# Performance work log

Hardware: AMD Instinct MI355X
Metric: run time of the kernel (lower is better)

## Reference

```python
import jax, jax.numpy as jnp
import numpy as np
import math

B, TD, TP, D, H = 16, 256, 1024, 512, 8
DH = D // H
G_MIN = 0.05
LN_EPS = 1e-5
SCALE = 1.0 / math.sqrt(DH)


def _ln(x, g, b):
    m = jnp.mean(x, axis=-1, keepdims=True)
    v = jnp.var(x, axis=-1, keepdims=True)
    return (x - m) * jax.lax.rsqrt(v + LN_EPS) * g + b


def _evi(x, w1, b1, w2, b2, k):
    # EvidentialHead: Linear -> SiLU -> Linear(d->4), NIG params -> gate
    h = jax.nn.silu(x @ w1 + b1)
    p = h @ w2 + b2  # (B,T,4)
    gamma, nu, alpha, beta = jnp.split(p, 4, axis=-1)
    nu = jax.nn.softplus(nu) + 1e-6
    alpha = jax.nn.softplus(alpha) + 1.0
    beta = jax.nn.softplus(beta) + 1e-6
    sigma2 = beta / (nu * (alpha - 1.0))  # (B,T,1)
    g = jnp.clip(jnp.exp(-k * sigma2[..., 0]), G_MIN, 1.0)  # (B,T)
    return g


def _xattn(Q, KV, log_bias, wq, bq, wk, bk, wv, bv, wo, bo, lng, lnb):
    # Q: (B,M,D), KV: (B,N,D), log_bias: (B,N) added to logits pre-softmax
    Bq, M, _ = Q.shape
    N = KV.shape[1]
    q = (Q @ wq + bq).reshape(Bq, M, H, DH)
    k_ = (KV @ wk + bk).reshape(Bq, N, H, DH)
    v = (KV @ wv + bv).reshape(Bq, N, H, DH)
    scores = jnp.einsum('bmhd,bnhd->bhmn', q, k_) * SCALE
    scores = scores + log_bias[:, None, None, :]
    attn = jax.nn.softmax(scores, axis=-1)
    out = jnp.einsum('bhmn,bnhd->bmhd', attn, v).reshape(Bq, M, D)
    out = out @ wo + bo
    return _ln(Q + out, lng, lnb)


def _ffn(x, w1, b1, w2, b2, lng, lnb):
    # Linear(d,4d) -> SiLU -> Linear(4d,d) -> LayerNorm (no residual)
    h = jax.nn.silu(x @ w1 + b1)
    return _ln(h @ w2 + b2, lng, lnb)


def setup_inputs() -> dict:
    key = jax.random.key(0)
    ks = iter(jax.random.split(key, 64))

    def w(shape, s=0.02):
        return s * jax.random.normal(next(ks), shape, jnp.float32)

    def attn_params(pfx):
        p = {}
        for nm in ('wq', 'wk', 'wv', 'wo'):
            p[pfx + '_' + nm] = w((D, D))
        for nm in ('bq', 'bk', 'bv', 'bo'):
            p[pfx + '_' + nm] = jnp.zeros((D,), jnp.float32)
        p[pfx + '_lng'] = jnp.ones((D,), jnp.float32)
        p[pfx + '_lnb'] = jnp.zeros((D,), jnp.float32)
        return p

    def ffn_params(pfx):
        return {pfx + '_w1': w((D, 4 * D)), pfx + '_b1': jnp.zeros((4 * D,), jnp.float32),
                pfx + '_w2': w((4 * D, D)), pfx + '_b2': jnp.zeros((D,), jnp.float32),
                pfx + '_lng': jnp.ones((D,), jnp.float32), pfx + '_lnb': jnp.zeros((D,), jnp.float32)}

    inp = {
        'Hd': jax.random.normal(next(ks), (B, TD, D), jnp.float32),
        'Hp': jax.random.normal(next(ks), (B, TP, D), jnp.float32),
        'k': 1,
        'evid_w1': w((D, D)), 'evid_b1': jnp.zeros((D,), jnp.float32),
        'evid_w2': w((D, 4)), 'evid_b2': jnp.zeros((4,), jnp.float32),
        'evip_w1': w((D, D)), 'evip_b1': jnp.zeros((D,), jnp.float32),
        'evip_w2': w((D, 4)), 'evip_b2': jnp.zeros((4,), jnp.float32),
    }
    inp.update(attn_params('p2d'))
    inp.update(attn_params('d2p'))
    inp.update(ffn_params('ffnd'))
    inp.update(ffn_params('ffnp'))
    return inp


def reference(Hd, Hp, k,
              evid_w1, evid_b1, evid_w2, evid_b2,
              evip_w1, evip_b1, evip_w2, evip_b2,
              p2d_wq, p2d_wk, p2d_wv, p2d_wo, p2d_bq, p2d_bk, p2d_bv, p2d_bo, p2d_lng, p2d_lnb,
              d2p_wq, d2p_wk, d2p_wv, d2p_wo, d2p_bq, d2p_bk, d2p_bv, d2p_bo, d2p_lng, d2p_lnb,
              ffnd_w1, ffnd_b1, ffnd_w2, ffnd_b2, ffnd_lng, ffnd_lnb,
              ffnp_w1, ffnp_b1, ffnp_w2, ffnp_b2, ffnp_lng, ffnp_lnb):
    gd = _evi(Hd, evid_w1, evid_b1, evid_w2, evid_b2, k)  # (B,TD)
    gp = _evi(Hp, evip_w1, evip_b1, evip_w2, evip_b2, k)  # (B,TP)
    Hp2 = _xattn(Hp, Hd, jnp.log(gd + 1e-12),
                 p2d_wq, p2d_bq, p2d_wk, p2d_bk, p2d_wv, p2d_bv, p2d_wo, p2d_bo, p2d_lng, p2d_lnb)
    Hd2 = _xattn(Hd, Hp, jnp.log(gp + 1e-12),
                 d2p_wq, d2p_bq, d2p_wk, d2p_bk, d2p_wv, d2p_bv, d2p_wo, d2p_bo, d2p_lng, d2p_lnb)
    Hd_out = _ffn(Hd2, ffnd_w1, ffnd_b1, ffnd_w2, ffnd_b2, ffnd_lng, ffnd_lnb)
    Hp_out = _ffn(Hp2, ffnp_w1, ffnp_b1, ffnp_w2, ffnp_b2, ffnp_lng, ffnp_lnb)
    return (Hd_out, Hp_out, gd, gp)
```

## Files before the change

kernel.cpp:

```cpp
#include <hip/hip_runtime.h>
#include <stdint.h>
#include <math.h>

typedef unsigned short u16;
typedef __attribute__((ext_vector_type(8))) short bf16x8;
typedef __attribute__((ext_vector_type(8))) short short8;
typedef __attribute__((ext_vector_type(4))) float f32x4;
typedef __attribute__((ext_vector_type(4))) unsigned short u16x4;

#define NB 16
#define TDr 256
#define TPr 1024
#define DM 512
#define NH 8
#define DHEAD 64

__device__ __forceinline__ float us2f(u16 u) {
  union { float f; unsigned int i; } x; x.i = ((unsigned int)u) << 16; return x.f;
}
__device__ __forceinline__ u16 f2us(float f) {
  union { float fl; unsigned int i; } x; x.fl = f;
  unsigned int u = x.i;
  return (u16)((u + 0x7fffu + ((u >> 16) & 1u)) >> 16);
}

__global__ __launch_bounds__(64) void detect_kernel(const u16* __restrict__ raw,
                                                    int* __restrict__ flag)
{
  const int lane = threadIdx.x;
  float mx = 0.f;
  for (int i = lane; i < 256; i += 64) {
    float v = us2f(raw[i]);
    v = fabsf(v);
    if (isfinite(v)) mx = fmaxf(mx, v); else mx = 1e30f;
  }
#pragma unroll
  for (int o = 32; o; o >>= 1) mx = fmaxf(mx, __shfl_xor(mx, o));
  if (lane == 0) flag[0] = (mx > 1e10f) ? 1 : 0;
}

struct CvtDesc { const void* src; unsigned long dst_off; int n; };
struct CvtTable { CvtDesc d[42]; };

__global__ __launch_bounds__(256) void cvt_kernel(CvtTable t, u16* __restrict__ base,
                                                  const int* __restrict__ flag)
{
  const CvtDesc d = t.d[blockIdx.y];
  u16* dst = base + d.dst_off;
  const int isf32 = flag[0];
  const int stride = gridDim.x * 256;
  const int tid0 = blockIdx.x * 256 + threadIdx.x;
  if (d.n >= 8) {
    const int n8 = d.n >> 3;
    if (isf32) {
      const float* s = (const float*)d.src;
      for (int i = tid0; i < n8; i += stride) {
        f32x4 a = *(const f32x4*)&s[i * 8];
        f32x4 b = *(const f32x4*)&s[i * 8 + 4];
        short8 o;
        o[0]=(short)f2us(a[0]); o[1]=(short)f2us(a[1]); o[2]=(short)f2us(a[2]); o[3]=(short)f2us(a[3]);
        o[4]=(short)f2us(b[0]); o[5]=(short)f2us(b[1]); o[6]=(short)f2us(b[2]); o[7]=(short)f2us(b[3]);
        *(short8*)&dst[i * 8] = o;
      }
    } else {
      const short8* s = (const short8*)d.src;
      for (int i = tid0; i < n8; i += stride) *(short8*)&dst[i * 8] = s[i];
    }
  } else {
    if (isf32) {
      const float* s = (const float*)d.src;
      for (int i = tid0; i < d.n; i += stride) dst[i] = f2us(s[i]);
    } else {
      const u16* s = (const u16*)d.src;
      for (int i = tid0; i < d.n; i += stride) dst[i] = s[i];
    }
  }
}

template<int BM, int BN>
__device__ __forceinline__ void gemm_core(
    const u16* __restrict__ Ab, const u16* __restrict__ Bb,
    int K, int tid, f32x4 (&acc)[BM/32][BN/32])
{
  constexpr int BK = 64;
  constexpr int FM = BM / 32;
  constexpr int FN = BN / 32;
  constexpr int CPT = BM * BK / 8 / 256;
  __shared__ __align__(16) u16 As[2][BM * BK];
  __shared__ __align__(16) u16 Bs[2][BN * BK];

  const int lane = tid & 63;
  const int wm = (tid >> 6) >> 1;
  const int wn = (tid >> 6) & 1;
  const int r16 = lane & 15;
  const int l4  = lane >> 4;

#pragma unroll
  for (int i = 0; i < FM; ++i)
#pragma unroll
    for (int j = 0; j < FN; ++j)
      acc[i][j] = (f32x4){0.f, 0.f, 0.f, 0.f};

  auto stage = [&](int buf, int k0) {
#pragma unroll
    for (int it = 0; it < CPT; ++it) {
      const int c = tid + it * 256;
      const int r = c >> 3;
      const int src = (c & 7) ^ (r & 7);
      __builtin_amdgcn_global_load_lds(
          (const __attribute__((address_space(1))) uint32_t*)(Ab + (long)r * K + k0 + src * 8),
          (__attribute__((address_space(3))) uint32_t*)(&As[buf][c * 8]), 16, 0, 0);
    }
#pragma unroll
    for (int it = 0; it < CPT; ++it) {
      const int c = tid + it * 256;
      const int r = c >> 3;
      const int src = (c & 7) ^ (r & 7);
      __builtin_amdgcn_global_load_lds(
          (const __attribute__((address_space(1))) uint32_t*)(Bb + (long)r * K + k0 + src * 8),
          (__attribute__((address_space(3))) uint32_t*)(&Bs[buf][c * 8]), 16, 0, 0);
    }
  };

  const int nt = K / BK;
  stage(0, 0);
  if (nt > 1) stage(1, BK);

  for (int t = 0; t < nt; ++t) {
    if (t + 1 < nt) {
      asm volatile("s_waitcnt vmcnt(8)" ::: "memory");
    } else {
      asm volatile("s_waitcnt vmcnt(0)" ::: "memory");
    }
    asm volatile("s_barrier" ::: "memory");
    __builtin_amdgcn_sched_barrier(0);

    const int cur = t & 1;
#pragma unroll
    for (int kh = 0; kh < 2; ++kh) {
      const int kc = kh * 4 + l4;
      bf16x8 af[FM], bfv[FN];
#pragma unroll
      for (int i = 0; i < FM; ++i) {
        const int row = wm * (BM/2) + i*16 + r16;
        af[i] = *(const bf16x8*)&As[cur][(row << 6) + ((kc ^ (row & 7)) << 3)];
      }
#pragma unroll
      for (int j = 0; j < FN; ++j) {
        const int row = wn * (BN/2) + j*16 + r16;
        bfv[j] = *(const bf16x8*)&Bs[cur][(row << 6) + ((kc ^ (row & 7)) << 3)];
      }
#pragma unroll
      for (int i = 0; i < FM; ++i)
#pragma unroll
        for (int j = 0; j < FN; ++j)
          acc[i][j] = __builtin_amdgcn_mfma_f32_16x16x32_bf16(af[i], bfv[j], acc[i][j], 0, 0, 0);
    }

    __builtin_amdgcn_sched_barrier(0);
    asm volatile("s_barrier" ::: "memory");
    __builtin_amdgcn_sched_barrier(0);
    if (t + 2 < nt) stage(cur, (t + 2) * BK);
  }
}

struct ProjSet {
  const u16 *A, *W, *bE, *bQ, *bK, *bV;
  u16 *H, *Q, *Kc, *VT;
  int ntokLog, mtiles;
};

__global__ __launch_bounds__(256) void proj_pair(ProjSet s0, ProjSet s1)
{
  const ProjSet S = blockIdx.z ? s1 : s0;
  if ((int)blockIdx.x >= S.mtiles) return;
  const int tid = threadIdx.x;
  const int lane = tid & 63;
  const int wm = (tid >> 6) >> 1, wn = (tid >> 6) & 1;
  const int r16 = lane & 15, rr4 = (lane >> 4) << 2;
  const long row0 = (long)blockIdx.x * 128;
  const long col0 = (long)blockIdx.y * 128;

  f32x4 acc[4][4];
  gemm_core<128,128>(S.A + row0 * 512, S.W + col0 * 512, 512, tid, acc);

  const int range = (int)(col0 >> 9);
  const u16* bp = range == 0 ? S.bE : range == 1 ? S.bQ : range == 2 ? S.bK : S.bV;
  u16* dst = range == 0 ? S.H : range == 1 ? S.Q : S.Kc;
  const int ntok = 1 << S.ntokLog;

#pragma unroll
  for (int i = 0; i < 4; ++i) {
    const long gr0 = row0 + wm*64 + i*16 + rr4;
#pragma unroll
    for (int j = 0; j < 4; ++j) {
      const int cr = (int)(col0 & 511) + wn*64 + j*16 + r16;
      const float badd = us2f(bp[cr]);
      if (range == 3) {
        const long b = gr0 >> S.ntokLog;
        const long t0 = gr0 & (ntok - 1);
        u16x4 pk;
#pragma unroll
        for (int r = 0; r < 4; ++r) pk[r] = f2us(acc[i][j][r] + badd);
        *(u16x4*)&S.VT[((long)b * 512 + cr) * ntok + t0] = pk;
      } else if (range == 0) {
#pragma unroll
        for (int r = 0; r < 4; ++r) {
          float v = acc[i][j][r] + badd;
          v = v / (1.f + __expf(-v));
          dst[(gr0 + r) * 512 + cr] = f2us(v);
        }
      } else {
#pragma unroll
        for (int r = 0; r < 4; ++r)
          dst[(gr0 + r) * 512 + cr] = f2us(acc[i][j][r] + badd);
      }
    }
  }
}

struct Gm { const u16* A; const u16* Bt; const u16* bias; u16* C; int mtiles; };

template<int SILU>
__global__ __launch_bounds__(256) void gemm_pair(Gm g0, Gm g1, int ldc, int K)
{
  const Gm G = blockIdx.z ? g1 : g0;
  if ((int)blockIdx.x >= G.mtiles) return;
  const int tid = threadIdx.x;
  const int lane = tid & 63;
  const int wm = (tid >> 6) >> 1, wn = (tid >> 6) & 1;
  const int r16 = lane & 15, rr4 = (lane >> 4) << 2;
  const long row0 = (long)blockIdx.x * 128;
  const long col0 = (long)blockIdx.y * 128;

  f32x4 acc[4][4];
  gemm_core<128,128>(G.A + row0 * (long)K, G.Bt + col0 * (long)K, K, tid, acc);

#pragma unroll
  for (int i = 0; i < 4; ++i) {
    const long gr0 = row0 + wm*64 + i*16 + rr4;
#pragma unroll
    for (int j = 0; j < 4; ++j) {
      const long gc = col0 + wn*64 + j*16 + r16;
      const float badd = us2f(G.bias[gc]);
#pragma unroll
      for (int r = 0; r < 4; ++r) {
        float v = acc[i][j][r] + badd;
        if (SILU) v = v / (1.f + __expf(-v));
        G.C[(gr0 + r) * (long)ldc + gc] = f2us(v);
      }
    }
  }
}

template<int NKV, int RPW>
__global__ __launch_bounds__(256) void attn_fused(
    const u16* __restrict__ Qp, const u16* __restrict__ Kp,
    const u16* __restrict__ Vt, const float* __restrict__ lb,
    u16* __restrict__ Aout, int M)
{
  constexpr int NC = NKV >> 7;
  constexpr int FI = RPW / 16;
  constexpr int NS = 4 * FI;
  constexpr int QT = 4 * RPW;
  constexpr int PLD = 136;
  __shared__ __align__(16) u16 Ps[4][RPW][PLD];

  const int tid  = threadIdx.x;
  const int lane = tid & 63;
  const int w    = tid >> 6;
  const int bh = blockIdx.y;
  const int b = bh >> 3, h = bh & 7;
  const long q0 = (long)blockIdx.x * QT;

  const u16* Qb = Qp + ((long)b * M + q0) * DM + h * DHEAD;
  const u16* Kb = Kp + (long)b * NKV * DM + h * DHEAD;
  const u16* Vb = Vt + ((long)b * DM + h * DHEAD) * NKV;
  const float* lbb = lb + (long)b * NKV;

  const int r16 = lane & 15;
  const int k8  = (lane >> 4) << 3;
  const int rr4 = (lane >> 4) << 2;
  const float SCALE = 0.125f;

  bf16x8 qa[FI][2];
#pragma unroll
  for (int i = 0; i < FI; ++i)
#pragma unroll
    for (int kc = 0; kc < 2; ++kc)
      qa[i][kc] = *(const bf16x8*)&Qb[(long)(w*RPW + i*16 + r16) * DM + kc*32 + k8];

  f32x4 acc_o[FI][4];
#pragma unroll
  for (int i = 0; i < FI; ++i)
#pragma unroll
    for (int jo = 0; jo < 4; ++jo)
      acc_o[i][jo] = (f32x4){0.f, 0.f, 0.f, 0.f};
  float mrow[NS], lrow[NS];
#pragma unroll
  for (int s = 0; s < NS; ++s) { mrow[s] = -1e30f; lrow[s] = 0.f; }

#pragma unroll
  for (int c = 0; c < NC; ++c) {
    const int t0 = c * 128;
    f32x4 acc_s[FI][8];
#pragma unroll
    for (int i = 0; i < FI; ++i)
#pragma unroll
      for (int j = 0; j < 8; ++j)
        acc_s[i][j] = (f32x4){0.f, 0.f, 0.f, 0.f};
#pragma unroll
    for (int j = 0; j < 8; ++j) {
      const long trow = t0 + j*16 + r16;
      bf16x8 kb0 = *(const bf16x8*)&Kb[trow * DM + k8];
      bf16x8 kb1 = *(const bf16x8*)&Kb[trow * DM + 32 + k8];
#pragma unroll
      for (int i = 0; i < FI; ++i) {
        acc_s[i][j] = __builtin_amdgcn_mfma_f32_16x16x32_bf16(qa[i][0], kb0, acc_s[i][j], 0, 0, 0);
        acc_s[i][j] = __builtin_amdgcn_mfma_f32_16x16x32_bf16(qa[i][1], kb1, acc_s[i][j], 0, 0, 0);
      }
    }

    float lbv[8];
#pragma unroll
    for (int j = 0; j < 8; ++j) lbv[j] = lbb[t0 + j*16 + r16];
    float pm[NS];
#pragma unroll
    for (int s = 0; s < NS; ++s) pm[s] = -1e30f;
#pragma unroll
    for (int i = 0; i < FI; ++i)
#pragma unroll
      for (int j = 0; j < 8; ++j)
#pragma unroll
        for (int r = 0; r < 4; ++r) {
          float v = acc_s[i][j][r] * SCALE + lbv[j];
          acc_s[i][j][r] = v;
          pm[i*4 + r] = fmaxf(pm[i*4 + r], v);
        }
#pragma unroll
    for (int s = 0; s < NS; ++s) {
#pragma unroll
      for (int o = 1; o < 16; o <<= 1) pm[s] = fmaxf(pm[s], __shfl_xor(pm[s], o));
    }
    float sc[NS];
#pragma unroll
    for (int s = 0; s < NS; ++s) {
      const float mn = fmaxf(mrow[s], pm[s]);
      sc[s] = __expf(mrow[s] - mn);
      mrow[s] = mn;
      lrow[s] *= sc[s];
    }
#pragma unroll
    for (int i = 0; i < FI; ++i)
#pragma unroll
      for (int jo = 0; jo < 4; ++jo)
#pragma unroll
        for (int r = 0; r < 4; ++r)
          acc_o[i][jo][r] *= sc[i*4 + r];

    float ls[NS];
#pragma unroll
    for (int s = 0; s < NS; ++s) ls[s] = 0.f;
#pragma unroll
    for (int i = 0; i < FI; ++i)
#pragma unroll
      for (int j = 0; j < 8; ++j)
#pragma unroll
        for (int r = 0; r < 4; ++r) {
          const float p = __expf(acc_s[i][j][r] - mrow[i*4 + r]);
          ls[i*4 + r] += p;
          Ps[w][i*16 + rr4 + r][j*16 + r16] = f2us(p);
        }
#pragma unroll
    for (int s = 0; s < NS; ++s) {
#pragma unroll
      for (int o = 1; o < 16; o <<= 1) ls[s] += __shfl_xor(ls[s], o);
      lrow[s] += ls[s];
    }

    asm volatile("s_waitcnt lgkmcnt(0)" ::: "memory");
    __builtin_amdgcn_sched_barrier(0);

#pragma unroll
    for (int kc = 0; kc < 4; ++kc) {
      bf16x8 pa[FI];
#pragma unroll
      for (int i = 0; i < FI; ++i)
        pa[i] = *(const bf16x8*)&Ps[w][i*16 + r16][kc*32 + k8];
#pragma unroll
      for (int jo = 0; jo < 4; ++jo) {
        bf16x8 vb = *(const bf16x8*)&Vb[(long)(jo*16 + r16) * NKV + t0 + kc*32 + k8];
#pragma unroll
        for (int i = 0; i < FI; ++i)
          acc_o[i][jo] = __builtin_amdgcn_mfma_f32_16x16x32_bf16(pa[i], vb, acc_o[i][jo], 0, 0, 0);
      }
    }
    __builtin_amdgcn_sched_barrier(0);
  }

  float linv[NS];
#pragma unroll
  for (int s = 0; s < NS; ++s) linv[s] = 1.f / lrow[s];
  u16* Ob = Aout + ((long)b * M + q0) * DM + h * DHEAD;
#pragma unroll
  for (int i = 0; i < FI; ++i)
#pragma unroll
    for (int jo = 0; jo < 4; ++jo)
#pragma unroll
      for (int r = 0; r < 4; ++r) {
        const long row = w*RPW + i*16 + rr4 + r;
        Ob[row * DM + jo*16 + r16] = f2us(acc_o[i][jo][r] * linv[i*4 + r]);
      }
}

struct TTab { const u16* in; u16* out; int R, C; };
struct TTable { TTab d[14]; };

__global__ __launch_bounds__(256) void transpose_all(TTable tt)
{
  const TTab d = tt.d[blockIdx.z];
  __shared__ u16 t[32][33];
  const int tx = threadIdx.x & 31, ty = threadIdx.x >> 5;
  for (int r0 = blockIdx.y * 32; r0 < d.R; r0 += gridDim.y * 32) {
    for (int c0 = blockIdx.x * 32; c0 < d.C; c0 += gridDim.x * 32) {
#pragma unroll
      for (int i = 0; i < 4; ++i)
        t[ty + 8*i][tx] = d.in[(long)(r0 + ty + 8*i) * d.C + c0 + tx];
      __syncthreads();
#pragma unroll
      for (int i = 0; i < 4; ++i)
        d.out[(long)(c0 + ty + 8*i) * d.R + r0 + tx] = t[tx][ty + 8*i];
      __syncthreads();
    }
  }
}

struct LnR { const u16* X; const u16* P; const u16* g; const u16* b; u16* out; int rows; };

__global__ __launch_bounds__(256) void ln_res_pair(LnR a0, LnR a1)
{
  const LnR A = blockIdx.z ? a1 : a0;
  const int row = blockIdx.x * 4 + (threadIdx.x >> 6);
  if (row >= A.rows) return;
  const int lane = threadIdx.x & 63;
  const u16* pr = A.P + (long)row * DM;
  const u16* xr = A.X + (long)row * DM;
  float v[8], s = 0.f, s2 = 0.f;
#pragma unroll
  for (int i = 0; i < 8; ++i) {
    const int jx = i * 64 + lane;
    float t = us2f(pr[jx]) + us2f(xr[jx]);
    v[i] = t; s += t; s2 += t * t;
  }
#pragma unroll
  for (int o = 32; o; o >>= 1) { s += __shfl_xor(s, o); s2 += __shfl_xor(s2, o); }
  const float mean = s * (1.f / DM);
  const float var  = s2 * (1.f / DM) - mean * mean;
  const float rstd = rsqrtf(fmaxf(var, 0.f) + 1e-5f);
#pragma unroll
  for (int i = 0; i < 8; ++i) {
    const int jx = i * 64 + lane;
    A.out[(long)row * DM + jx] = f2us((v[i] - mean) * rstd * us2f(A.g[jx]) + us2f(A.b[jx]));
  }
}

struct LnF { const u16* P; const u16* g; const u16* b; long oofs; int rows; };

__global__ __launch_bounds__(256) void ln_final_pair(LnF a0, LnF a1,
                                                     void* __restrict__ outb,
                                                     const int* __restrict__ flag)
{
  const LnF A = blockIdx.z ? a1 : a0;
  const int row = blockIdx.x * 4 + (threadIdx.x >> 6);
  if (row >= A.rows) return;
  const int lane = threadIdx.x & 63;
  const u16* pr = A.P + (long)row * DM;
  float v[8], s = 0.f, s2 = 0.f;
#pragma unroll
  for (int i = 0; i < 8; ++i) {
    const int jx = i * 64 + lane;
    float t = us2f(pr[jx]);
    v[i] = t; s += t; s2 += t * t;
  }
#pragma unroll
  for (int o = 32; o; o >>= 1) { s += __shfl_xor(s, o); s2 += __shfl_xor(s2, o); }
  const float mean = s * (1.f / DM);
  const float var  = s2 * (1.f / DM) - mean * mean;
  const float rstd = rsqrtf(fmaxf(var, 0.f) + 1e-5f);
  const int isf32 = flag[0];
#pragma unroll
  for (int i = 0; i < 8; ++i) {
    const int jx = i * 64 + lane;
    const float ov = (v[i] - mean) * rstd * us2f(A.g[jx]) + us2f(A.b[jx]);
    if (isf32) ((float*)outb)[A.oofs + (long)row * DM + jx] = ov;
    else       ((u16*)outb)[A.oofs + (long)row * DM + jx] = f2us(ov);
  }
}

struct Gt { const u16* H; const u16* W2; const u16* b2; long oofs; float* lb; int rows; };

__global__ __launch_bounds__(256) void gate_pair(Gt a0, Gt a1,
                                                 const int* __restrict__ kptr,
                                                 void* __restrict__ outb,
                                                 const int* __restrict__ flag)
{
  const Gt A = blockIdx.z ? a1 : a0;
  const int row = blockIdx.x * 4 + (threadIdx.x >> 6);
  if (row >= A.rows) return;
  const int lane = threadIdx.x & 63;
  const u16* hr = A.H + (long)row * DM;
  float p1 = 0.f, p2 = 0.f, p3 = 0.f;
#pragma unroll
  for (int i = 0; i < 8; ++i) {
    const int idx = i * 64 + lane;
    const float hv = us2f(hr[idx]);
    const u16x4 w = *(const u16x4*)&A.W2[idx * 4];
    p1 += hv * us2f(w[1]);
    p2 += hv * us2f(w[2]); p3 += hv * us2f(w[3]);
  }
#pragma unroll
  for (int o = 32; o; o >>= 1) {
    p1 += __shfl_xor(p1, o);
    p2 += __shfl_xor(p2, o); p3 += __shfl_xor(p3, o);
  }
  if (lane == 0) {
    const float nu = p1 + us2f(A.b2[1]);
    const float al = p2 + us2f(A.b2[2]);
    const float be = p3 + us2f(A.b2[3]);
    auto sp = [](float x) { return x > 20.f ? x : log1pf(expf(x)); };
    const float spn = sp(nu) + 1e-6f;
    const float spa = sp(al);
    const float spb = sp(be) + 1e-6f;
    const float sig = spb / (spn * spa);
    const float kk = (float)kptr[0];
    float gg = expf(-kk * sig);
    gg = fminf(fmaxf(gg, 0.05f), 1.f);
    if (flag[0]) ((float*)outb)[A.oofs + row] = gg;
    else         ((u16*)outb)[A.oofs + row] = f2us(gg);
    A.lb[row] = logf(gg + 1e-12f);
  }
}

extern "C" void kernel_launch(void* const* d_in, const int* in_sizes, int n_in,
                              void* d_out, int out_size, void* d_ws, size_t ws_size,
                              hipStream_t stream)
{
  const int* kptr = (const int*)d_in[2];

  uint8_t* base = (uint8_t*)d_ws;
  size_t off = 0;
  auto take = [&](size_t bytes) -> void* {
    void* p = base + off;
    off += (bytes + 255) & ~(size_t)255;
    return p;
  };
  int* FLAG = (int*)take(256);

  const int sizes[42] = {
    2097152, 8388608,
    262144, 512, 2048, 4,
    262144, 512, 2048, 4,
    262144,262144,262144,262144, 512,512,512,512, 512,512,
    262144,262144,262144,262144, 512,512,512,512, 512,512,
    1048576, 2048, 1048576, 512, 512, 512,
    1048576, 2048, 1048576, 512, 512, 512
  };
  u16* canon[42];
  u16* cbase = (u16*)take(17319944ul * 2 + 256);
  {
    unsigned long coff = 0;
    for (int i = 0; i < 42; ++i) {
      canon[i] = cbase + coff;
      coff += (unsigned long)((sizes[i] + 7) & ~7);
    }
  }
  const u16 *HdC = canon[0], *HpC = canon[1];
  const u16 *evid_w1 = canon[2], *evid_b1 = canon[3], *evid_w2 = canon[4], *evid_b2 = canon[5];
  const u16 *evip_w1 = canon[6], *evip_b1 = canon[7], *evip_w2 = canon[8], *evip_b2 = canon[9];
  const u16 *p2d_wq = canon[10], *p2d_wk = canon[11], *p2d_wv = canon[12], *p2d_wo = canon[13];
  const u16 *p2d_bq = canon[14], *p2d_bk = canon[15], *p2d_bv = canon[16], *p2d_bo = canon[17];
  const u16 *p2d_lng = canon[18], *p2d_lnb = canon[19];
  const u16 *d2p_wq = canon[20], *d2p_wk = canon[21], *d2p_wv = canon[22], *d2p_wo = canon[23];
  const u16 *d2p_bq = canon[24], *d2p_bk = canon[25], *d2p_bv = canon[26], *d2p_bo = canon[27];
  const u16 *d2p_lng = canon[28], *d2p_lnb = canon[29];
  const u16 *ffnd_w1 = canon[30], *ffnd_b1 = canon[31], *ffnd_w2 = canon[32], *ffnd_b2 = canon[33];
  const u16 *ffnd_lng = canon[34], *ffnd_lnb = canon[35];
  const u16 *ffnp_w1 = canon[36], *ffnp_b1 = canon[37], *ffnp_w2 = canon[38], *ffnp_b2 = canon[39];
  const u16 *ffnp_lng = canon[40], *ffnp_lnb = canon[41];

  u16* HpW = (u16*)take((size_t)2048*512*2);
  u16* HdW = (u16*)take((size_t)2048*512*2);
  u16* woT_p = (u16*)take((size_t)512*512*2);
  u16* woT_d = (u16*)take((size_t)512*512*2);
  u16* ffnp_w1T = (u16*)take((size_t)2048*512*2);
  u16* ffnp_w2T = (u16*)take((size_t)512*2048*2);
  u16* ffnd_w1T = (u16*)take((size_t)2048*512*2);
  u16* ffnd_w2T = (u16*)take((size_t)512*2048*2);

  u16* HBUF_p = (u16*)take((size_t)16384*512*2);
  u16* HBUF_d = (u16*)take((size_t)4096*512*2);
  u16* QBUF_p = (u16*)take((size_t)16384*512*2);
  u16* QBUF_d = (u16*)take((size_t)4096*512*2);
  u16* KBUF_p = (u16*)take((size_t)16384*512*2);
  u16* KBUF_d = (u16*)take((size_t)4096*512*2);
  u16* VT_p   = (u16*)take((size_t)16384*512*2);
  u16* VT_d   = (u16*)take((size_t)4096*512*2);
  u16* ABUF_p = (u16*)take((size_t)16384*512*2);
  u16* ABUF_d = (u16*)take((size_t)4096*512*2);
  u16* HP2  = (u16*)take((size_t)16384*512*2);
  u16* HD2  = (u16*)take((size_t)4096*512*2);
  float* LBD  = (float*)take((size_t)NB*TDr*4);
  float* LBP  = (float*)take((size_t)NB*TPr*4);
  if (off > ws_size) return;

  u16* PBUF_p = HBUF_p;
  u16* PBUF_d = HBUF_d;
  u16* SBUF_p = QBUF_p;
  u16* SBUF_d = SBUF_p + (size_t)16384*2048;

  const long O_HD = 0;
  const long O_HP = 2097152;
  const long O_GD = 10485760;
  const long O_GP = 10489856;

  detect_kernel<<<dim3(1), 64, 0, stream>>>((const u16*)d_in[0], FLAG);
  CvtTable tbl;
  {
    int ii = 0;
    for (int i = 0; i < 43; ++i) {
      if (i == 2) continue;
      tbl.d[ii].src = d_in[i];
      tbl.d[ii].dst_off = (unsigned long)(canon[ii] - cbase);
      tbl.d[ii].n = sizes[ii];
      ++ii;
    }
  }
  cvt_kernel<<<dim3(64, 42), 256, 0, stream>>>(tbl, cbase, FLAG);

  TTable tt;
  {
    const TTab tts[14] = {
      {evip_w1, HpW + 0*512*512, 512, 512},
      {p2d_wq,  HpW + 1*512*512, 512, 512},
      {d2p_wk,  HpW + 2*512*512, 512, 512},
      {d2p_wv,  HpW + 3*512*512, 512, 512},
      {evid_w1, HdW + 0*512*512, 512, 512},
      {d2p_wq,  HdW + 1*512*512, 512, 512},
      {p2d_wk,  HdW + 2*512*512, 512, 512},
      {p2d_wv,  HdW + 3*512*512, 512, 512},
      {p2d_wo, woT_p, 512, 512}, {d2p_wo, woT_d, 512, 512},
      {ffnp_w1, ffnp_w1T, 512, 2048}, {ffnp_w2, ffnp_w2T, 2048, 512},
      {ffnd_w1, ffnd_w1T, 512, 2048}, {ffnd_w2, ffnd_w2T, 2048, 512},
    };
    for (int i = 0; i < 14; ++i) tt.d[i] = tts[i];
  }
  transpose_all<<<dim3(16, 16, 14), 256, 0, stream>>>(tt);

  ProjSet sp{HpC, HpW, evip_b1, p2d_bq, d2p_bk, d2p_bv,
             HBUF_p, QBUF_p, KBUF_p, VT_p, 10, 128};
  ProjSet sd{HdC, HdW, evid_b1, d2p_bq, p2d_bk, p2d_bv,
             HBUF_d, QBUF_d, KBUF_d, VT_d, 8, 32};
  proj_pair<<<dim3(128, 16, 2), 256, 0, stream>>>(sp, sd);

  Gt gp{HBUF_p, evip_w2, evip_b2, O_GP, LBP, 16384};
  Gt gd{HBUF_d, evid_w2, evid_b2, O_GD, LBD, 4096};
  gate_pair<<<dim3(4096, 1, 2), 256, 0, stream>>>(gp, gd, kptr, d_out, FLAG);

  attn_fused<TDr,32><<<dim3(TPr/128, NB*NH), 256, 0, stream>>>(
      QBUF_p, KBUF_d, VT_d, LBD, ABUF_p, TPr);
  attn_fused<TPr,16><<<dim3(TDr/64, NB*NH), 256, 0, stream>>>(
      QBUF_d, KBUF_p, VT_p, LBP, ABUF_d, TDr);

  Gm wp{ABUF_p, woT_p, p2d_bo, PBUF_p, 128};
  Gm wd{ABUF_d, woT_d, d2p_bo, PBUF_d, 32};
  gemm_pair<0><<<dim3(128, 4, 2), 256, 0, stream>>>(wp, wd, 512, 512);

  LnR lp{HpC, PBUF_p, p2d_lng, p2d_lnb, HP2, 16384};
  LnR ld{HdC, PBUF_d, d2p_lng, d2p_lnb, HD2, 4096};
  ln_res_pair<<<dim3(4096, 1, 2), 256, 0, stream>>>(lp, ld);

  Gm f1p{HP2, ffnp_w1T, ffnp_b1, SBUF_p, 128};
  Gm f1d{HD2, ffnd_w1T, ffnd_b1, SBUF_d, 32};
  gemm_pair<1><<<dim3(128, 16, 2), 256, 0, stream>>>(f1p, f1d, 2048, 512);

  Gm f2p{SBUF_p, ffnp_w2T, ffnp_b2, PBUF_p, 128};
  Gm f2d{SBUF_d, ffnd_w2T, ffnd_b2, PBUF_d, 32};
  gemm_pair<0><<<dim3(128, 4, 2), 256, 0, stream>>>(f2p, f2d, 512, 2048);

  LnF fp{PBUF_p, ffnp_lng, ffnp_lnb, O_HP, 16384};
  LnF fd{PBUF_d, ffnd_lng, ffnd_lnb, O_HD, 4096};
  ln_final_pair<<<dim3(4096, 1, 2), 256, 0, stream>>>(fp, fd, d_out, FLAG);
}
```

Measured before the change: 451.8 us.

## Switch GEMMs to 256x256 tiles with 8 waves and XCD-aware block swizzle

Replaces the 128x128 four-wave GEMM core with a 256x256 eight-wave core. Each wave holds a 128x64 accumulator block and loads the B fragments once per K step. Stage prefetch now happens right after a barrier, MFMA bursts are wrapped in s_setprio, and block IDs are remapped so neighbouring tiles land on the same XCD. The larger tiles aim to raise arithmetic intensity and L2 reuse across the projection and FFN GEMMs. In exchange they cut the grid size (the d-branch gets only 16 M-tiles), use 128KB of LDS per block, and raise register pressure.

```diff
diff --git a/kernel.cpp b/kernel.cpp
--- a/kernel.cpp
+++ b/kernel.cpp
@@ -77,34 +77,27 @@
   }
 }
 
-template<int BM, int BN>
-__device__ __forceinline__ void gemm_core(
+__device__ __forceinline__ void gemm256_core(
     const u16* __restrict__ Ab, const u16* __restrict__ Bb,
-    int K, int tid, f32x4 (&acc)[BM/32][BN/32])
-{
-  constexpr int BK = 64;
-  constexpr int FM = BM / 32;
-  constexpr int FN = BN / 32;
-  constexpr int CPT = BM * BK / 8 / 256;
-  __shared__ __align__(16) u16 As[2][BM * BK];
-  __shared__ __align__(16) u16 Bs[2][BN * BK];
-
+    int K, int tid, f32x4 (&acc)[8][4])
+{
+  __shared__ __align__(16) u16 As[2][256 * 64];
+  __shared__ __align__(16) u16 Bs[2][256 * 64];
   const int lane = tid & 63;
-  const int wm = (tid >> 6) >> 1;
-  const int wn = (tid >> 6) & 1;
-  const int r16 = lane & 15;
-  const int l4  = lane >> 4;
-
-#pragma unroll
-  for (int i = 0; i < FM; ++i)
-#pragma unroll
-    for (int j = 0; j < FN; ++j)
+  const int wid = tid >> 6;
+  const int wm = wid >> 2, wn = wid & 3;
+  const int r16 = lane & 15, l4 = lane >> 4;
+
+#pragma unroll
+  for (int i = 0; i < 8; ++i)
+#pragma unroll
+    for (int j = 0; j < 4; ++j)
       acc[i][j] = (f32x4){0.f, 0.f, 0.f, 0.f};
 
   auto stage = [&](int buf, int k0) {
 #pragma unroll
-    for (int it = 0; it < CPT; ++it) {
-      const int c = tid + it * 256;
+    for (int it = 0; it < 4; ++it) {
+      const int c = tid + it * 512;
       const int r = c >> 3;
       const int src = (c & 7) ^ (r & 7);
       __builtin_amdgcn_global_load_lds(
@@ -112,8 +105,8 @@
           (__attribute__((address_space(3))) uint32_t*)(&As[buf][c * 8]), 16, 0, 0);
     }
 #pragma unroll
-    for (int it = 0; it < CPT; ++it) {
-      const int c = tid + it * 256;
+    for (int it = 0; it < 4; ++it) {
+      const int c = tid + it * 512;
       const int r = c >> 3;
       const int src = (c & 7) ^ (r & 7);
       __builtin_amdgcn_global_load_lds(
@@ -122,12 +115,14 @@
     }
   };
 
-  const int nt = K / BK;
+  const int nt = K >> 6;
   stage(0, 0);
-  if (nt > 1) stage(1, BK);
 
   for (int t = 0; t < nt; ++t) {
+    const int cur = t & 1;
+    asm volatile("s_barrier" ::: "memory");
     if (t + 1 < nt) {
+      stage(cur ^ 1, (t + 1) << 6);
       asm volatile("s_waitcnt vmcnt(8)" ::: "memory");
     } else {
       asm volatile("s_waitcnt vmcnt(0)" ::: "memory");
@@ -135,33 +130,53 @@
     asm volatile("s_barrier" ::: "memory");
     __builtin_amdgcn_sched_barrier(0);
 
-    const int cur = t & 1;
-#pragma unroll
-    for (int kh = 0; kh < 2; ++kh) {
-      const int kc = kh * 4 + l4;
-      bf16x8 af[FM], bfv[FN];
-#pragma unroll
-      for (int i = 0; i < FM; ++i) {
-        const int row = wm * (BM/2) + i*16 + r16;
-        af[i] = *(const bf16x8*)&As[cur][(row << 6) + ((kc ^ (row & 7)) << 3)];
+    bf16x8 bf[4][2];
+#pragma unroll
+    for (int q = 0; q < 4; ++q) {
+      bf16x8 af[2][2];
+#pragma unroll
+      for (int mi = 0; mi < 2; ++mi) {
+        const int row = wm * 128 + (2 * q + mi) * 16 + r16;
+#pragma unroll
+        for (int kk = 0; kk < 2; ++kk) {
+          const int kc = kk * 4 + l4;
+          af[mi][kk] = *(const bf16x8*)&As[cur][(row << 6) + ((kc ^ (row & 7)) << 3)];
+        }
       }
-#pragma unroll
-      for (int j = 0; j < FN; ++j) {
-        const int row = wn * (BN/2) + j*16 + r16;
-        bfv[j] = *(const bf16x8*)&Bs[cur][(row << 6) + ((kc ^ (row & 7)) << 3)];
+      if (q == 0) {
+#pragma unroll
+        for (int j = 0; j < 4; ++j) {
+          const int rowb = wn * 64 + j * 16 + r16;
+#pragma unroll
+          for (int kk = 0; kk < 2; ++kk) {
+            const int kc = kk * 4 + l4;
+            bf[j][kk] = *(const bf16x8*)&Bs[cur][(rowb << 6) + ((kc ^ (rowb & 7)) << 3)];
+          }
+        }
       }
-#pragma unroll
-      for (int i = 0; i < FM; ++i)
-#pragma unroll
-        for (int j = 0; j < FN; ++j)
-          acc[i][j] = __builtin_amdgcn_mfma_f32_16x16x32_bf16(af[i], bfv[j], acc[i][j], 0, 0, 0);
-    }
-
-    __builtin_amdgcn_sched_barrier(0);
-    asm volatile("s_barrier" ::: "memory");
-    __builtin_amdgcn_sched_barrier(0);
-    if (t + 2 < nt) stage(cur, (t + 2) * BK);
-  }
+      asm volatile("s_waitcnt lgkmcnt(0)" ::: "memory");
+      __builtin_amdgcn_sched_barrier(0);
+      __builtin_amdgcn_s_setprio(1);
+#pragma unroll
+      for (int mi = 0; mi < 2; ++mi)
+#pragma unroll
+        for (int j = 0; j < 4; ++j)
+#pragma unroll
+          for (int kk = 0; kk < 2; ++kk)
+            acc[2 * q + mi][j] = __builtin_amdgcn_mfma_f32_16x16x32_bf16(
+                af[mi][kk], bf[j][kk], acc[2 * q + mi][j], 0, 0, 0);
+      __builtin_amdgcn_s_setprio(0);
+    }
+  }
+}
+
+__device__ __forceinline__ void xcd_swz(int& bx, int& by, int gy)
+{
+  const int nwg = 64 * gy;
+  const int bid = by * 64 + bx;
+  const int s = (bid & 7) * (nwg >> 3) + (bid >> 3);
+  bx = s & 63;
+  by = s >> 6;
 }
 
 struct ProjSet {
@@ -170,50 +185,53 @@
   int ntokLog, mtiles;
 };
 
-__global__ __launch_bounds__(256) void proj_pair(ProjSet s0, ProjSet s1)
+__global__ __launch_bounds__(512, 2) void proj_pair(ProjSet s0, ProjSet s1)
 {
   const ProjSet S = blockIdx.z ? s1 : s0;
-  if ((int)blockIdx.x >= S.mtiles) return;
+  int bx = blockIdx.x, by = blockIdx.y;
+  xcd_swz(bx, by, gridDim.y);
+  if (bx >= S.mtiles) return;
   const int tid = threadIdx.x;
+
+  f32x4 acc[8][4];
+  gemm256_core(S.A + (long)bx * 256 * 512, S.W + (long)by * 256 * 512, 512, tid, acc);
+
   const int lane = tid & 63;
-  const int wm = (tid >> 6) >> 1, wn = (tid >> 6) & 1;
+  const int wid = tid >> 6;
+  const int wm = wid >> 2, wn = wid & 3;
   const int r16 = lane & 15, rr4 = (lane >> 4) << 2;
-  const long row0 = (long)blockIdx.x * 128;
-  const long col0 = (long)blockIdx.y * 128;
-
-  f32x4 acc[4][4];
-  gemm_core<128,128>(S.A + row0 * 512, S.W + col0 * 512, 512, tid, acc);
-
-  const int range = (int)(col0 >> 9);
+  const long row0 = (long)bx * 256 + wm * 128;
+  const long colB = (long)by * 256;
+  const int range = (int)(colB >> 9);
   const u16* bp = range == 0 ? S.bE : range == 1 ? S.bQ : range == 2 ? S.bK : S.bV;
   u16* dst = range == 0 ? S.H : range == 1 ? S.Q : S.Kc;
   const int ntok = 1 << S.ntokLog;
 
 #pragma unroll
-  for (int i = 0; i < 4; ++i) {
-    const long gr0 = row0 + wm*64 + i*16 + rr4;
+  for (int fi = 0; fi < 8; ++fi) {
+    const long gr0 = row0 + fi * 16 + rr4;
 #pragma unroll
     for (int j = 0; j < 4; ++j) {
-      const int cr = (int)(col0 & 511) + wn*64 + j*16 + r16;
+      const int cr = (int)(colB & 511) + wn * 64 + j * 16 + r16;
       const float badd = us2f(bp[cr]);
       if (range == 3) {
         const long b = gr0 >> S.ntokLog;
         const long t0 = gr0 & (ntok - 1);
         u16x4 pk;
 #pragma unroll
-        for (int r = 0; r < 4; ++r) pk[r] = f2us(acc[i][j][r] + badd);
+        for (int r = 0; r < 4; ++r) pk[r] = f2us(acc[fi][j][r] + badd);
         *(u16x4*)&S.VT[((long)b * 512 + cr) * ntok + t0] = pk;
       } else if (range == 0) {
 #pragma unroll
         for (int r = 0; r < 4; ++r) {
-          float v = acc[i][j][r] + badd;
+          float v = acc[fi][j][r] + badd;
           v = v / (1.f + __expf(-v));
           dst[(gr0 + r) * 512 + cr] = f2us(v);
         }
       } else {
 #pragma unroll
         for (int r = 0; r < 4; ++r)
-          dst[(gr0 + r) * 512 + cr] = f2us(acc[i][j][r] + badd);
+          dst[(gr0 + r) * 512 + cr] = f2us(acc[fi][j][r] + badd);
       }
     }
   }
@@ -222,30 +240,34 @@
 struct Gm { const u16* A; const u16* Bt; const u16* bias; u16* C; int mtiles; };
 
 template<int SILU>
-__global__ __launch_bounds__(256) void gemm_pair(Gm g0, Gm g1, int ldc, int K)
+__global__ __launch_bounds__(512, 2) void gemm_pair(Gm g0, Gm g1, int ldc, int K)
 {
   const Gm G = blockIdx.z ? g1 : g0;
-  if ((int)blockIdx.x >= G.mtiles) return;
+  int bx = blockIdx.x, by = blockIdx.y;
+  xcd_swz(bx, by, gridDim.y);
+  if (bx >= G.mtiles) return;
   const int tid = threadIdx.x;
+
+  f32x4 acc[8][4];
+  gemm256_core(G.A + (long)bx * 256 * K, G.Bt + (long)by * 256 * K, K, tid, acc);
+
   const int lane = tid & 63;
-  const int wm = (tid >> 6) >> 1, wn = (tid >> 6) & 1;
+  const int wid = tid >> 6;
+  const int wm = wid >> 2, wn = wid & 3;
   const int r16 = lane & 15, rr4 = (lane >> 4) << 2;
-  const long row0 = (long)blockIdx.x * 128;
-  const long col0 = (long)blockIdx.y * 128;
-
-  f32x4 acc[4][4];
-  gemm_core<128,128>(G.A + row0 * (long)K, G.Bt + col0 * (long)K, K, tid, acc);
-
-#pragma unroll
-  for (int i = 0; i < 4; ++i) {
-    const long gr0 = row0 + wm*64 + i*16 + rr4;
+  const long row0 = (long)bx * 256 + wm * 128;
+  const long col0 = (long)by * 256 + wn * 64;
+
+#pragma unroll
+  for (int fi = 0; fi < 8; ++fi) {
+    const long gr0 = row0 + fi * 16 + rr4;
 #pragma unroll
     for (int j = 0; j < 4; ++j) {
-      const long gc = col0 + wn*64 + j*16 + r16;
+      const long gc = col0 + j * 16 + r16;
       const float badd = us2f(G.bias[gc]);
 #pragma unroll
       for (int r = 0; r < 4; ++r) {
-        float v = acc[i][j][r] + badd;
+        float v = acc[fi][j][r] + badd;
         if (SILU) v = v / (1.f + __expf(-v));
         G.C[(gr0 + r) * (long)ldc + gc] = f2us(v);
       }
@@ -657,10 +679,10 @@
   transpose_all<<<dim3(16, 16, 14), 256, 0, stream>>>(tt);
 
   ProjSet sp{HpC, HpW, evip_b1, p2d_bq, d2p_bk, d2p_bv,
-             HBUF_p, QBUF_p, KBUF_p, VT_p, 10, 128};
+             HBUF_p, QBUF_p, KBUF_p, VT_p, 10, 64};
   ProjSet sd{HdC, HdW, evid_b1, d2p_bq, p2d_bk, p2d_bv,
-             HBUF_d, QBUF_d, KBUF_d, VT_d, 8, 32};
-  proj_pair<<<dim3(128, 16, 2), 256, 0, stream>>>(sp, sd);
+             HBUF_d, QBUF_d, KBUF_d, VT_d, 8, 16};
+  proj_pair<<<dim3(64, 8, 2), 512, 0, stream>>>(sp, sd);
 
   Gt gp{HBUF_p, evip_w2, evip_b2, O_GP, LBP, 16384};
   Gt gd{HBUF_d, evid_w2, evid_b2, O_GD, LBD, 4096};
@@ -671,21 +693,21 @@
   attn_fused<TPr,16><<<dim3(TDr/64, NB*NH), 256, 0, stream>>>(
       QBUF_d, KBUF_p, VT_p, LBP, ABUF_d, TDr);
 
-  Gm wp{ABUF_p, woT_p, p2d_bo, PBUF_p, 128};
-  Gm wd{ABUF_d, woT_d, d2p_bo, PBUF_d, 32};
-  gemm_pair<0><<<dim3(128, 4, 2), 256, 0, stream>>>(wp, wd, 512, 512);
+  Gm wp{ABUF_p, woT_p, p2d_bo, PBUF_p, 64};
+  Gm wd{ABUF_d, woT_d, d2p_bo, PBUF_d, 16};
+  gemm_pair<0><<<dim3(64, 2, 2), 512, 0, stream>>>(wp, wd, 512, 512);
 
   LnR lp{HpC, PBUF_p, p2d_lng, p2d_lnb, HP2, 16384};
   LnR ld{HdC, PBUF_d, d2p_lng, d2p_lnb, HD2, 4096};
   ln_res_pair<<<dim3(4096, 1, 2), 256, 0, stream>>>(lp, ld);
 
-  Gm f1p{HP2, ffnp_w1T, ffnp_b1, SBUF_p, 128};
-  Gm f1d{HD2, ffnd_w1T, ffnd_b1, SBUF_d, 32};
-  gemm_pair<1><<<dim3(128, 16, 2), 256, 0, stream>>>(f1p, f1d, 2048, 512);
-
-  Gm f2p{SBUF_p, ffnp_w2T, ffnp_b2, PBUF_p, 128};
-  Gm f2d{SBUF_d, ffnd_w2T, ffnd_b2, PBUF_d, 32};
-  gemm_pair<0><<<dim3(128, 4, 2), 256, 0, stream>>>(f2p, f2d, 512, 2048);
+  Gm f1p{HP2, ffnp_w1T, ffnp_b1, SBUF_p, 64};
+  Gm f1d{HD2, ffnd_w1T, ffnd_b1, SBUF_d, 16};
+  gemm_pair<1><<<dim3(64, 8, 2), 512, 0, stream>>>(f1p, f1d, 2048, 512);
+
+  Gm f2p{SBUF_p, ffnp_w2T, ffnp_b2, PBUF_p, 64};
+  Gm f2d{SBUF_d, ffnd_w2T, ffnd_b2, PBUF_d, 16};
+  gemm_pair<0><<<dim3(64, 2, 2), 512, 0, stream>>>(f2p, f2d, 512, 2048);
 
   LnF fp{PBUF_p, ffnp_lng, ffnp_lnb, O_HP, 16384};
   LnF fd{PBUF_d, ffnd_lng, ffnd_lnb, O_HD, 4096};
```

Measured after the change: 496.0 us. 9.8% more time.
